# Kernel tuning notes

Measured on AMD Instinct MI355X. Metric: run time of the kernel, lower is better.

Reference implementation:

```python
import jax, jax.numpy as jnp
import numpy as np

N_NODES = 50000
N_EDGES = 800000
F_IN = 32
H = 128
N_REL = 4
MAX_DEG = 10
N_GRAPHS = 64
N_BLOCKS = 2


def setup_inputs() -> dict:
    key = jax.random.key(0)
    ks = jax.random.split(key, 20)
    s = 0.05
    return {
        "x": jax.random.normal(ks[0], (N_NODES, F_IN), jnp.float32),
        "edge_index": jax.random.randint(ks[1], (2, N_EDGES), 0, N_NODES, dtype=jnp.int32),
        "edge_attr": jax.random.randint(ks[2], (N_EDGES,), 0, N_REL, dtype=jnp.int32),
        "batch_idx": jnp.sort(jax.random.randint(ks[3], (N_NODES,), 0, N_GRAPHS, dtype=jnp.int32)),
        "embed_W": jax.random.normal(ks[4], (F_IN, H), jnp.float32) * s,
        "embed_b": jax.random.normal(ks[5], (H,), jnp.float32) * s,
        "rgcn_Wrel": jax.random.normal(ks[6], (N_BLOCKS, N_REL, H, H), jnp.float32) * s,
        "rgcn_Wroot": jax.random.normal(ks[7], (N_BLOCKS, H, H), jnp.float32) * s,
        "rgcn_b": jax.random.normal(ks[8], (N_BLOCKS, H), jnp.float32) * s,
        "mf_Wl": jax.random.normal(ks[9], (N_BLOCKS, MAX_DEG + 1, H, H), jnp.float32) * s,
        "mf_bl": jax.random.normal(ks[10], (N_BLOCKS, MAX_DEG + 1, H), jnp.float32) * s,
        "mf_Wr": jax.random.normal(ks[11], (N_BLOCKS, MAX_DEG + 1, H, H), jnp.float32) * s,
        "lin1_W": jax.random.normal(ks[12], (H, H), jnp.float32) * s,
        "lin1_b": jax.random.normal(ks[13], (H,), jnp.float32) * s,
        "lin2_W": jax.random.normal(ks[14], (H, 1), jnp.float32) * s,
        "lin2_b": jax.random.normal(ks[15], (1,), jnp.float32) * s,
    }


def _rgcn(x, src, dst, rel, Wrel, Wroot, b):
    # PyG RGCNConv with default aggr='mean': per-relation mean over incoming
    # edges, then per-relation weight, plus root transform and bias.
    seg = dst * N_REL + rel  # composite segment id: (node, relation)
    agg = jax.ops.segment_sum(x[src], seg, num_segments=N_NODES * N_REL)
    cnt = jax.ops.segment_sum(jnp.ones((seg.shape[0],), x.dtype), seg,
                              num_segments=N_NODES * N_REL)
    agg = (agg / jnp.maximum(cnt, 1.0)[:, None]).reshape(N_NODES, N_REL, H)
    return jnp.einsum('nrh,rho->no', agg, Wrel) + x @ Wroot + b


def _mfconv(x, src, dst, Wl, bl, Wr):
    # PyG MFConv: sum-aggregate neighbors, then per-degree-bucket linear heads
    # (degree = in-degree clamped to MAX_DEG); lin_r applied to root x (no bias).
    h = jax.ops.segment_sum(x[src], dst, num_segments=N_NODES)  # [N,H]
    deg = jax.ops.segment_sum(jnp.ones((src.shape[0],), jnp.int32), dst,
                              num_segments=N_NODES)
    deg = jnp.minimum(deg, MAX_DEG)  # [N]
    # out_all: [D+1, N, H] candidate outputs, one per degree bucket
    out_all = (jnp.einsum('nh,dho->dno', h, Wl)
               + jnp.einsum('nh,dho->dno', x, Wr)
               + bl[:, None, :])
    return jnp.take_along_axis(out_all, deg[None, :, None], axis=0)[0]


def reference(x, edge_index, edge_attr, batch_idx, embed_W, embed_b,
              rgcn_Wrel, rgcn_Wroot, rgcn_b, mf_Wl, mf_bl, mf_Wr,
              lin1_W, lin1_b, lin2_W, lin2_b):
    src, dst = edge_index[0], edge_index[1]
    h = x @ embed_W + embed_b
    for blk in range(N_BLOCKS):
        if blk > 0:  # first block uses Identity instead of ReLU
            h = jax.nn.relu(h)
        h = _rgcn(h, src, dst, edge_attr, rgcn_Wrel[blk], rgcn_Wroot[blk], rgcn_b[blk])
        h = jax.nn.relu(h)
        h = _mfconv(h, src, dst, mf_Wl[blk], mf_bl[blk], mf_Wr[blk])
    g = jax.ops.segment_sum(h, batch_idx, num_segments=N_GRAPHS)  # global_add_pool
    g = jax.nn.relu(g @ lin1_W + lin1_b)
    return g @ lin2_W + lin2_b
```

## Files before the change

kernel.cpp:

```cpp
#include <hip/hip_runtime.h>
#include <hip/hip_bf16.h>

#define NRELS 4
#define MAXDEG 10
#define NBUCK 11
#define POOL_CHUNKS 8

typedef __attribute__((ext_vector_type(8))) short s16x8;
typedef __attribute__((ext_vector_type(4))) float f32x4;
typedef __attribute__((ext_vector_type(8))) unsigned short u16x8;

__device__ inline unsigned short f2b(float f) {
  __hip_bfloat16 h = __float2bfloat16(f);
  return *reinterpret_cast<unsigned short*>(&h);
}
__device__ inline float b2f(unsigned short u) {
  union { unsigned int i; float f; } v;
  v.i = ((unsigned int)u) << 16;
  return v.f;
}
__device__ inline float blo(unsigned int v) {
  union { unsigned int i; float f; } x;
  x.i = v << 16;
  return x.f;
}
__device__ inline float bhi(unsigned int v) {
  union { unsigned int i; float f; } x;
  x.i = v & 0xffff0000u;
  return x.f;
}

typedef __attribute__((address_space(3))) unsigned int lds_uint;
typedef __attribute__((address_space(1))) const unsigned int glob_uint;
__device__ __forceinline__ void gld_lds16(const void* g, void* l) {
  __builtin_amdgcn_global_load_lds((glob_uint*)g, (lds_uint*)l, 16, 0, 0);
}

__global__ __launch_bounds__(512) void coarse_count_scan(
    const int* __restrict__ dst, int* __restrict__ bhist, int* __restrict__ boff,
    int* __restrict__ bcur, int* __restrict__ done, int* __restrict__ perm, int permCap,
    int NB, int E, int nblocks) {
  __shared__ int lh[512];
  __shared__ int lastf;
  int t = threadIdx.x;
  lh[t] = 0;
  __syncthreads();
  for (int i = blockIdx.x * 512 + t; i < permCap; i += nblocks * 512) perm[i] = -1;
  int base = blockIdx.x * 4096;
  int lim = E - base;
  if (lim > 4096) lim = 4096;
  for (int i = t; i < lim; i += 512) atomicAdd(&lh[dst[base + i] >> 7], 1);
  __syncthreads();
  if (lh[t]) atomicAdd(&bhist[t], lh[t]);
  __threadfence();
  __syncthreads();
  if (t == 0) lastf = (atomicAdd(done, 1) == nblocks - 1) ? 1 : 0;
  __syncthreads();
  if (!lastf) return;
  int v = (t < NB) ? atomicAdd(&bhist[t], 0) : 0;
  lh[t] = v;
  __syncthreads();
  for (int o = 1; o < 512; o <<= 1) {
    int x = (t >= o) ? lh[t - o] : 0;
    __syncthreads();
    lh[t] += x;
    __syncthreads();
  }
  if (t < NB) {
    int st = lh[t] - v;
    boff[t] = st;
    bcur[t] = st;
  }
  if (t == 0) boff[NB] = E;
}

__global__ __launch_bounds__(512) void coarse_scatter(
    const int* __restrict__ src, const int* __restrict__ dst, const int* __restrict__ rel,
    int* __restrict__ bcur, uint2* __restrict__ ebuf, int E) {
  __shared__ int lhist[512];
  __shared__ int lstart[512];
  __shared__ int lcur[512];
  __shared__ int gbase[512];
  __shared__ uint2 stage[4096];
  int t = threadIdx.x;
  lhist[t] = 0;
  __syncthreads();
  int base = blockIdx.x * 4096;
  int lim = E - base;
  if (lim > 4096) lim = 4096;
  for (int i = t; i < lim; i += 512) atomicAdd(&lhist[dst[base + i] >> 7], 1);
  __syncthreads();
  int myc = lhist[t];
  lstart[t] = myc;
  __syncthreads();
  for (int o = 1; o < 512; o <<= 1) {
    int x = (t >= o) ? lstart[t - o] : 0;
    __syncthreads();
    lstart[t] += x;
    __syncthreads();
  }
  int incl = lstart[t];
  __syncthreads();
  lstart[t] = incl - myc;
  lcur[t] = 0;
  if (myc > 0) gbase[t] = atomicAdd(&bcur[t], myc);
  __syncthreads();
  for (int i = t; i < lim; i += 512) {
    int e = base + i;
    int d = dst[e];
    int b = d >> 7;
    int slot = lstart[b] + atomicAdd(&lcur[b], 1);
    stage[slot] = make_uint2((unsigned)(d * 4 + rel[e]), (unsigned)src[e]);
  }
  __syncthreads();
  for (int i = t; i < lim; i += 512) {
    uint2 val = stage[i];
    int b = (int)(val.x >> 9);
    ebuf[gbase[b] + (i - lstart[b])] = val;
  }
}

__global__ __launch_bounds__(512) void fine_place(
    const uint2* __restrict__ ebuf, const int* __restrict__ boff, int* __restrict__ cnt,
    int* __restrict__ seg_start, float* __restrict__ inv, int* __restrict__ deg,
    int* __restrict__ bucket, int* __restrict__ hist, int* __restrict__ csr, int NSEG) {
  __shared__ int lh[512];
  __shared__ int sc[512];
  __shared__ int lcur[512];
  __shared__ int lbh[16];
  int t = threadIdx.x;
  int b = blockIdx.x;
  lh[t] = 0;
  if (t < 16) lbh[t] = 0;
  __syncthreads();
  int s = boff[b], e = boff[b + 1];
  for (int i = s + t; i < e; i += 512) atomicAdd(&lh[ebuf[i].x & 511], 1);
  __syncthreads();
  int v = lh[t];
  sc[t] = v;
  __syncthreads();
  for (int o = 1; o < 512; o <<= 1) {
    int x = (t >= o) ? sc[t - o] : 0;
    __syncthreads();
    sc[t] += x;
    __syncthreads();
  }
  int gseg = b * 512 + t;
  int mystart = s + sc[t] - v;
  lcur[t] = mystart;
  if (gseg < NSEG) {
    cnt[gseg] = v;
    seg_start[gseg] = mystart;
    inv[gseg] = 1.0f / (float)(v > 1 ? v : 1);
    if ((t & 3) == 0) {
      int d = sc[t + 3] - sc[t] + v;
      int n = gseg >> 2;
      deg[n] = d;
      int bk = d < MAXDEG ? d : MAXDEG;
      bucket[n] = bk;
      atomicAdd(&lbh[bk], 1);
    }
  }
  __syncthreads();
  if (t < NBUCK && lbh[t]) atomicAdd(&hist[t], lbh[t]);
  for (int i = s + t; i < e; i += 512) {
    uint2 vv = ebuf[i];
    int pos = atomicAdd(&lcur[vv.x & 511], 1);
    csr[pos] = (int)vv.y;
  }
}

__global__ void build_perm(const int* __restrict__ bucket, const int* __restrict__ hist,
                           int* __restrict__ fill, int* __restrict__ perm, int N) {
  __shared__ int soff[NBUCK];
  if (threadIdx.x == 0) {
    int acc = 0;
    for (int b = 0; b < NBUCK; b++) {
      soff[b] = acc;
      acc += ((hist[b] + 63) >> 6) << 6;
    }
  }
  __syncthreads();
  int n = blockIdx.x * 256 + threadIdx.x;
  int b = (n < N) ? bucket[n] : -1;
  int lane = threadIdx.x & 63;
  for (int bb = 0; bb < NBUCK; bb++) {
    unsigned long long m = __ballot(b == bb);
    if (m == 0ULL) continue;
    int leader = __ffsll(m) - 1;
    int base = 0;
    if (lane == leader) base = atomicAdd(&fill[bb], __popcll(m));
    base = __shfl(base, leader);
    if (b == bb) {
      int idx = __popcll(m & ((1ULL << lane) - 1ULL));
      perm[soff[bb] + base + idx] = n;
    }
  }
}

__global__ __launch_bounds__(256) void embed_conv(
    const float* __restrict__ x, const float* __restrict__ embW,
    const float* __restrict__ bias, const float* __restrict__ Wrel,
    const float* __restrict__ Wroot, const float* __restrict__ Wl,
    const float* __restrict__ Wr, unsigned short* __restrict__ Bt,
    unsigned short* __restrict__ Btm, unsigned short* __restrict__ out, int N, int nbE) {
  if ((int)blockIdx.x >= nbE) {
    const int R1 = 2 * 128 * 640;
    const int R2 = R1 + 2 * 11 * 128 * 256;
    int t = (blockIdx.x - nbE) * 256 + threadIdx.x;
    if (t < R1) {
      int blk = t / 81920;
      int rem = t % 81920;
      int n = rem / 640;
      int k = rem % 640;
      float v;
      if (k < 512)
        v = Wrel[(size_t)blk * 65536 + (size_t)k * 128 + n];
      else
        v = Wroot[(size_t)blk * 16384 + (size_t)(k - 512) * 128 + n];
      Bt[t] = f2b(v);
    } else if (t < R2) {
      int t2 = t - R1;
      int k = t2 & 255;
      int n = (t2 >> 8) & 127;
      int bb = (t2 >> 15) % 11;
      int blk = t2 / (11 * 128 * 256);
      float v;
      if (k < 128)
        v = Wl[(((size_t)blk * 11 + bb) * 128 + k) * 128 + n];
      else
        v = Wr[(((size_t)blk * 11 + bb) * 128 + (k - 128)) * 128 + n];
      Btm[t2] = f2b(v);
    }
    return;
  }
  __shared__ unsigned char As[64 * 80];
  __shared__ unsigned char Bs[128 * 80];
  int t = threadIdx.x;
  int m0 = blockIdx.x * 64;
  {
    int r = t >> 2, s = t & 3;
    int gr = m0 + r;
    if (gr >= N) gr = N - 1;
    const float* xp = x + (size_t)gr * 32 + s * 8;
    float4 f0 = *(const float4*)xp;
    float4 f1 = *(const float4*)(xp + 4);
    u16x8 o;
    o[0] = f2b(f0.x); o[1] = f2b(f0.y); o[2] = f2b(f0.z); o[3] = f2b(f0.w);
    o[4] = f2b(f1.x); o[5] = f2b(f1.y); o[6] = f2b(f1.z); o[7] = f2b(f1.w);
    *(u16x8*)(As + r * 80 + s * 16) = o;
  }
  {
    int n = t >> 1, hf = t & 1;
    unsigned short tmp[16];
#pragma unroll
    for (int j = 0; j < 16; j++) tmp[j] = f2b(embW[(size_t)(hf * 16 + j) * 128 + n]);
    *(u16x8*)(Bs + n * 80 + hf * 32) = *(u16x8*)tmp;
    *(u16x8*)(Bs + n * 80 + hf * 32 + 16) = *(u16x8*)(tmp + 8);
  }
  __syncthreads();
  int lane = t & 63, wave = t >> 6;
  int row = lane & 15, quad = lane >> 4;
  int nh = wave * 32;
  f32x4 acc[2][4];
#pragma unroll
  for (int i = 0; i < 2; i++)
#pragma unroll
    for (int j = 0; j < 4; j++) acc[i][j] = (f32x4){0.f, 0.f, 0.f, 0.f};
  s16x8 af[4], bf[2];
#pragma unroll
  for (int mt = 0; mt < 4; mt++) {
    int R = mt * 16 + row;
    af[mt] = *(const s16x8*)(As + R * 80 + quad * 16);
  }
#pragma unroll
  for (int nt = 0; nt < 2; nt++) {
    int R = nh + nt * 16 + row;
    bf[nt] = *(const s16x8*)(Bs + R * 80 + quad * 16);
  }
#pragma unroll
  for (int nt = 0; nt < 2; nt++)
#pragma unroll
    for (int mt = 0; mt < 4; mt++)
      acc[nt][mt] = __builtin_amdgcn_mfma_f32_16x16x32_bf16(af[mt], bf[nt], acc[nt][mt], 0, 0, 0);
#pragma unroll
  for (int nt = 0; nt < 2; nt++) {
    int n = nh + nt * 16 + row;
    float bv = bias[n];
#pragma unroll
    for (int mt = 0; mt < 4; mt++) {
#pragma unroll
      for (int r4 = 0; r4 < 4; r4++) {
        int m = m0 + mt * 16 + quad * 4 + r4;
        if (m < N) out[(size_t)m * 128 + n] = f2b(acc[nt][mt][r4] + bv);
      }
    }
  }
}

__device__ __forceinline__ void acc8v(float* a, uint4 v) {
  a[0] += blo(v.x); a[1] += bhi(v.x);
  a[2] += blo(v.y); a[3] += bhi(v.y);
  a[4] += blo(v.z); a[5] += bhi(v.z);
  a[6] += blo(v.w); a[7] += bhi(v.w);
}

__device__ __forceinline__ void gather_seg(const unsigned short* __restrict__ hb,
                                           const int* __restrict__ csr, int st, int cn,
                                           int chunk, float* a) {
  const unsigned short* hq = hb + chunk * 16;
  int i = 0;
  for (; i + 2 <= cn; i += 2) {
    int p0 = csr[st + i], p1 = csr[st + i + 1];
    const uint4* r0 = (const uint4*)(hq + (size_t)p0 * 128);
    const uint4* r1 = (const uint4*)(hq + (size_t)p1 * 128);
    uint4 v00 = r0[0], v01 = r0[1];
    uint4 v10 = r1[0], v11 = r1[1];
    acc8v(a + 0, v00); acc8v(a + 8, v01);
    acc8v(a + 0, v10); acc8v(a + 8, v11);
  }
  if (i < cn) {
    const uint4* r0 = (const uint4*)(hq + (size_t)csr[st + i] * 128);
    acc8v(a + 0, r0[0]); acc8v(a + 8, r0[1]);
  }
}

__device__ __forceinline__ void write_frag(unsigned char* Ag, int ln, int chunk,
                                           const float* a, float w) {
  int s = chunk >> 2;
#pragma unroll
  for (int h = 0; h < 2; h++) {
    int c = (((chunk & 3) * 2 + h)) ^ (ln & 7);
    const float* p = a + h * 8;
    uint4 o;
    o.x = (unsigned int)f2b(p[0] * w) | ((unsigned int)f2b(p[1] * w) << 16);
    o.y = (unsigned int)f2b(p[2] * w) | ((unsigned int)f2b(p[3] * w) << 16);
    o.z = (unsigned int)f2b(p[4] * w) | ((unsigned int)f2b(p[5] * w) << 16);
    o.w = (unsigned int)f2b(p[6] * w) | ((unsigned int)f2b(p[7] * w) << 16);
    *(uint4*)(Ag + s * 8192 + ln * 128 + (c << 4)) = o;
  }
}

__device__ __forceinline__ void gemm_tile_gB(const unsigned char* Areg, const char* Bp,
                                             int strideB, int row, int quad, int nh,
                                             f32x4 acc[2][4]) {
#pragma unroll
  for (int s = 0; s < 2; s++) {
#pragma unroll
    for (int ks = 0; ks < 2; ks++) {
      int cch = ks * 4 + quad;
      s16x8 af[4], bf[2];
#pragma unroll
      for (int mt = 0; mt < 4; mt++) {
        int R = mt * 16 + row;
        af[mt] = *(const s16x8*)(Areg + s * 8192 + R * 128 + ((cch ^ (R & 7)) << 4));
      }
#pragma unroll
      for (int nt = 0; nt < 2; nt++) {
        int R = nh + nt * 16 + row;
        bf[nt] = *(const s16x8*)(Bp + (size_t)R * strideB + s * 128 + cch * 16);
      }
#pragma unroll
      for (int nt = 0; nt < 2; nt++)
#pragma unroll
        for (int mt = 0; mt < 4; mt++)
          acc[nt][mt] = __builtin_amdgcn_mfma_f32_16x16x32_bf16(af[mt], bf[nt], acc[nt][mt], 0, 0, 0);
    }
  }
}

__global__ __launch_bounds__(256) void rgcn_fused(
    const unsigned short* __restrict__ hb, const int* __restrict__ csr,
    const int* __restrict__ seg_start, const int* __restrict__ cnt,
    const float* __restrict__ inv, const int* __restrict__ perm,
    const unsigned short* __restrict__ Bt, const float* __restrict__ bias,
    unsigned short* __restrict__ out) {
  __shared__ unsigned char Ag[16384];
  __shared__ int nodes[64];
  int t = threadIdx.x;
  int m0 = blockIdx.x * 64;
  if (t < 64) nodes[t] = perm[m0 + t];
  __syncthreads();
  int lane = t & 63, wave = t >> 6;
  int row = lane & 15, quad = lane >> 4;
  int nh = wave * 32;
  int chunk = t & 7, lnb = t >> 3;
  f32x4 acc[2][4];
#pragma unroll
  for (int i = 0; i < 2; i++)
#pragma unroll
    for (int j = 0; j < 4; j++) acc[i][j] = (f32x4){0.f, 0.f, 0.f, 0.f};

  for (int rel = 0; rel < 4; rel++) {
#pragma unroll
    for (int pp = 0; pp < 2; pp++) {
      int ln = pp * 32 + lnb;
      int nd = nodes[ln];
      float a[16];
#pragma unroll
      for (int j = 0; j < 16; j++) a[j] = 0.f;
      float w = 1.f;
      if (nd >= 0) {
        int sid = nd * 4 + rel;
        int st = seg_start[sid], cn2 = cnt[sid];
        w = inv[sid];
        gather_seg(hb, csr, st, cn2, chunk, a);
      }
      write_frag(Ag, ln, chunk, a, w);
    }
    __syncthreads();
    gemm_tile_gB(Ag, (const char*)Bt + rel * 256, 1280, row, quad, nh, acc);
    __syncthreads();
  }
#pragma unroll
  for (int s = 0; s < 2; s++)
#pragma unroll
    for (int p = 0; p < 2; p++) {
      int o = s * 8192 + p * 4096 + t * 16;
      int r = (o >> 7) & 63, c = ((o >> 4) & 7) ^ (r & 7);
      int nd = nodes[r];
      if (nd < 0) nd = 0;
      gld_lds16((const char*)hb + (size_t)nd * 256 + s * 128 + c * 16, Ag + o);
    }
  __syncthreads();
  gemm_tile_gB(Ag, (const char*)Bt + 1024, 1280, row, quad, nh, acc);
#pragma unroll
  for (int nt = 0; nt < 2; nt++) {
    int n = nh + nt * 16 + row;
    float bv = bias[n];
#pragma unroll
    for (int mt = 0; mt < 4; mt++) {
#pragma unroll
      for (int r4 = 0; r4 < 4; r4++) {
        int nd = nodes[mt * 16 + quad * 4 + r4];
        if (nd >= 0) out[(size_t)nd * 128 + n] = f2b(fmaxf(acc[nt][mt][r4] + bv, 0.f));
      }
    }
  }
}

__global__ __launch_bounds__(256) void mf_fused(
    const unsigned short* __restrict__ hb, const int* __restrict__ csr,
    const int* __restrict__ seg_start, const int* __restrict__ deg,
    const int* __restrict__ perm, const int* __restrict__ hist,
    const unsigned short* __restrict__ Bt, const float* __restrict__ bl,
    unsigned short* __restrict__ out, int relu_out) {
  __shared__ unsigned char Ag[16384];
  __shared__ int nodes[64];
  __shared__ int soff[NBUCK + 1];
  int t = threadIdx.x;
  int m0 = blockIdx.x * 64;
  if (t == 0) {
    int a2 = 0;
    for (int b2 = 0; b2 < NBUCK; b2++) {
      soff[b2] = a2;
      a2 += ((hist[b2] + 63) >> 6) << 6;
    }
    soff[NBUCK] = a2;
  }
  if (t < 64) nodes[t] = perm[m0 + t];
  __syncthreads();
  if (m0 >= soff[NBUCK]) return;
  int b = 0;
  while (b < 10 && m0 >= soff[b + 1]) b++;
  const char* Bb = (const char*)(Bt + (size_t)b * 128 * 256);
  int lane = t & 63, wave = t >> 6;
  int row = lane & 15, quad = lane >> 4;
  int nh = wave * 32;
  int chunk = t & 7, lnb = t >> 3;
  f32x4 acc[2][4];
#pragma unroll
  for (int i = 0; i < 2; i++)
#pragma unroll
    for (int j = 0; j < 4; j++) acc[i][j] = (f32x4){0.f, 0.f, 0.f, 0.f};
#pragma unroll
  for (int pp = 0; pp < 2; pp++) {
    int ln = pp * 32 + lnb;
    int nd = nodes[ln];
    float a[16];
#pragma unroll
    for (int j = 0; j < 16; j++) a[j] = 0.f;
    if (nd >= 0) gather_seg(hb, csr, seg_start[nd * 4], deg[nd], chunk, a);
    write_frag(Ag, ln, chunk, a, 1.f);
  }
  __syncthreads();
  gemm_tile_gB(Ag, Bb, 512, row, quad, nh, acc);
  __syncthreads();
#pragma unroll
  for (int s = 0; s < 2; s++)
#pragma unroll
    for (int p = 0; p < 2; p++) {
      int o = s * 8192 + p * 4096 + t * 16;
      int r = (o >> 7) & 63, c = ((o >> 4) & 7) ^ (r & 7);
      int nd = nodes[r];
      if (nd < 0) nd = 0;
      gld_lds16((const char*)hb + (size_t)nd * 256 + s * 128 + c * 16, Ag + o);
    }
  __syncthreads();
  gemm_tile_gB(Ag, Bb + 256, 512, row, quad, nh, acc);
  const float* bb = bl + b * 128;
#pragma unroll
  for (int nt = 0; nt < 2; nt++) {
    int n = nh + nt * 16 + row;
    float bv = bb[n];
#pragma unroll
    for (int mt = 0; mt < 4; mt++) {
#pragma unroll
      for (int r4 = 0; r4 < 4; r4++) {
        int nd = nodes[mt * 16 + quad * 4 + r4];
        if (nd >= 0) {
          float v = acc[nt][mt][r4] + bv;
          if (relu_out) v = fmaxf(v, 0.f);
          out[(size_t)nd * 128 + n] = f2b(v);
        }
      }
    }
  }
}

__global__ void pool2(const unsigned short* __restrict__ h, const int* __restrict__ batch,
                      float* __restrict__ g, int N, int G) {
  int gr = blockIdx.x / POOL_CHUNKS;
  int ck = blockIdx.x % POOL_CHUNKS;
  int t = threadIdx.x;
  int lane = t & 63, grp = t >> 6;
  int lo = 0, hi = N;
  while (lo < hi) {
    int m = (lo + hi) >> 1;
    if (batch[m] < gr) lo = m + 1; else hi = m;
  }
  int s = lo;
  lo = s; hi = N;
  while (lo < hi) {
    int m = (lo + hi) >> 1;
    if (batch[m] < gr + 1) lo = m + 1; else hi = m;
  }
  int e = lo;
  int len = e - s;
  int a = s + (int)(((long long)len * ck) / POOL_CHUNKS);
  int b = s + (int)(((long long)len * (ck + 1)) / POOL_CHUNKS);
  float s0 = 0.f, s1 = 0.f;
  for (int n = a + grp; n < b; n += 2) {
    unsigned int v = *(const unsigned int*)(h + (size_t)n * 128 + lane * 2);
    s0 += blo(v);
    s1 += bhi(v);
  }
  if (b > a + grp) {
    atomicAdd(&g[gr * 128 + lane * 2], s0);
    atomicAdd(&g[gr * 128 + lane * 2 + 1], s1);
  }
}

__global__ void head_kernel(const float* __restrict__ g, const float* __restrict__ W1,
                            const float* __restrict__ b1, const float* __restrict__ W2,
                            const float* __restrict__ b2, float* __restrict__ out) {
  int bg = blockIdx.x;
  int o = threadIdx.x;
  __shared__ float gs[128];
  __shared__ float red[128];
  gs[o] = g[bg * 128 + o];
  __syncthreads();
  float acc = b1[o];
  for (int k = 0; k < 128; k++) acc += gs[k] * W1[k * 128 + o];
  acc = fmaxf(acc, 0.f);
  red[o] = acc * W2[o];
  __syncthreads();
  for (int s = 64; s > 0; s >>= 1) {
    if (o < s) red[o] += red[o + s];
    __syncthreads();
  }
  if (o == 0) out[bg] = red[0] + b2[0];
}

extern "C" void kernel_launch(void* const* d_in, const int* in_sizes, int n_in,
                              void* d_out, int out_size, void* d_ws, size_t ws_size,
                              hipStream_t stream) {
  const float* x = (const float*)d_in[0];
  const int* ei = (const int*)d_in[1];
  const int* ea = (const int*)d_in[2];
  const int* batch = (const int*)d_in[3];
  const float* embW = (const float*)d_in[4];
  const float* embB = (const float*)d_in[5];
  const float* Wrel = (const float*)d_in[6];
  const float* Wroot = (const float*)d_in[7];
  const float* rb = (const float*)d_in[8];
  const float* Wl = (const float*)d_in[9];
  const float* bl = (const float*)d_in[10];
  const float* Wr = (const float*)d_in[11];
  const float* l1W = (const float*)d_in[12];
  const float* l1b = (const float*)d_in[13];
  const float* l2W = (const float*)d_in[14];
  const float* l2b = (const float*)d_in[15];
  float* out = (float*)d_out;

  int N = in_sizes[0] / 32;
  int E = in_sizes[2];
  int G = out_size;
  int NSEG = N * 4;
  int NB = (N + 127) >> 7;

  char* p = (char*)d_ws;
  auto alloc = [&](size_t bytes) {
    char* r = p;
    p += (bytes + 255) & ~(size_t)255;
    return r;
  };
  int permCap = ((N + 63) / 64 + NBUCK) * 64;
  unsigned short* h_bf = (unsigned short*)alloc((size_t)N * 128 * 2);
  unsigned short* h2_bf = (unsigned short*)alloc((size_t)N * 128 * 2);
  unsigned short* Btr = (unsigned short*)alloc((size_t)2 * 128 * 640 * 2);
  unsigned short* Btm = (unsigned short*)alloc((size_t)2 * 11 * 128 * 256 * 2);
  float* inv = (float*)alloc((size_t)NSEG * 4);
  int* cnt = (int*)alloc((size_t)NSEG * 4);
  int* seg_start = (int*)alloc((size_t)NSEG * 4);
  int* csr = (int*)alloc((size_t)E * 4);
  uint2* ebuf = (uint2*)alloc((size_t)E * 8);
  int* deg = (int*)alloc((size_t)N * 4);
  int* bucket = (int*)alloc((size_t)N * 4);
  int* perm = (int*)alloc((size_t)permCap * 4);
  int* boff = (int*)alloc(516 * 4);
  int* bcur = (int*)alloc(512 * 4);
  size_t zeroBytes = 8192 + (size_t)G * 128 * 4;
  char* zb = alloc(zeroBytes);
  int* bhist = (int*)zb;
  int* hist = (int*)(zb + 4096);
  int* fill = (int*)(zb + 4224);
  int* done = (int*)(zb + 4352);
  float* g = (float*)(zb + 8192);

  (void)hipMemsetAsync(zb, 0, zeroBytes, stream);

  const int* src = ei;
  const int* dst = ei + E;

  int sblocks = (E + 4095) / 4096;
  coarse_count_scan<<<sblocks, 512, 0, stream>>>(dst, bhist, boff, bcur, done, perm, permCap,
                                                 NB, E, sblocks);
  coarse_scatter<<<sblocks, 512, 0, stream>>>(src, dst, ea, bcur, ebuf, E);
  fine_place<<<NB, 512, 0, stream>>>(ebuf, boff, cnt, seg_start, inv, deg, bucket, hist, csr,
                                     NSEG);
  build_perm<<<(N + 255) / 256, 256, 0, stream>>>(bucket, hist, fill, perm, N);

  int nbE = (N + 63) / 64;
  int convBlocks = (2 * 128 * 640 + 2 * 11 * 128 * 256 + 255) / 256;
  embed_conv<<<nbE + convBlocks, 256, 0, stream>>>(x, embW, embB, Wrel, Wroot, Wl, Wr, Btr,
                                                   Btm, h_bf, N, nbE);

  int mfblocks = permCap / 64;
  for (int blk = 0; blk < 2; blk++) {
    rgcn_fused<<<mfblocks, 256, 0, stream>>>(h_bf, csr, seg_start, cnt, inv, perm,
                                             Btr + (size_t)blk * 81920, rb + blk * 128,
                                             h2_bf);
    mf_fused<<<mfblocks, 256, 0, stream>>>(h2_bf, csr, seg_start, deg, perm, hist,
                                           Btm + (size_t)blk * 11 * 128 * 256,
                                           bl + (size_t)blk * 11 * 128, h_bf,
                                           (blk == 0) ? 1 : 0);
  }
  pool2<<<G * POOL_CHUNKS, 128, 0, stream>>>(h_bf, batch, g, N, G);
  head_kernel<<<G, 128, 0, stream>>>(g, l1W, l1b, l2W, l2b, out);
}
```

Before: 406.2 us.

## Double LDS buffers to overlap neighbor gathers and root-row loads with GEMMs

In the RGCN kernel, two relations are gathered per iteration into separate LDS buffers, so one barrier pair covers two GEMM tiles and the segment metadata is read with vector loads. In the MFConv kernel, the async root-row load into a second LDS buffer is issued before the neighbor gather, and both GEMMs run after a single barrier. This cuts barrier count and hides global-load latency behind gather work. In exchange, LDS use per block doubles to about 32KB and register pressure rises from two live accumulator arrays, which may lower occupancy.

```diff
diff --git a/kernel.cpp b/kernel.cpp
--- a/kernel.cpp
+++ b/kernel.cpp
@@ -375,7 +375,8 @@
     const float* __restrict__ inv, const int* __restrict__ perm,
     const unsigned short* __restrict__ Bt, const float* __restrict__ bias,
     unsigned short* __restrict__ out) {
-  __shared__ unsigned char Ag[16384];
+  __shared__ unsigned char Ag0[16384];
+  __shared__ unsigned char Ag1[16384];
   __shared__ int nodes[64];
   int t = threadIdx.x;
   int m0 = blockIdx.x * 64;
@@ -391,25 +392,31 @@
 #pragma unroll
     for (int j = 0; j < 4; j++) acc[i][j] = (f32x4){0.f, 0.f, 0.f, 0.f};
 
-  for (int rel = 0; rel < 4; rel++) {
+#pragma unroll
+  for (int rp = 0; rp < 4; rp += 2) {
 #pragma unroll
     for (int pp = 0; pp < 2; pp++) {
       int ln = pp * 32 + lnb;
       int nd = nodes[ln];
-      float a[16];
-#pragma unroll
-      for (int j = 0; j < 16; j++) a[j] = 0.f;
-      float w = 1.f;
+      float a0[16], a1[16];
+#pragma unroll
+      for (int j = 0; j < 16; j++) { a0[j] = 0.f; a1[j] = 0.f; }
+      float w0 = 1.f, w1 = 1.f;
       if (nd >= 0) {
-        int sid = nd * 4 + rel;
-        int st = seg_start[sid], cn2 = cnt[sid];
-        w = inv[sid];
-        gather_seg(hb, csr, st, cn2, chunk, a);
+        int sb = nd * 4 + rp;
+        int2 st2 = *(const int2*)(seg_start + sb);
+        int2 cn2 = *(const int2*)(cnt + sb);
+        float2 w2 = *(const float2*)(inv + sb);
+        w0 = w2.x; w1 = w2.y;
+        gather_seg(hb, csr, st2.x, cn2.x, chunk, a0);
+        gather_seg(hb, csr, st2.y, cn2.y, chunk, a1);
       }
-      write_frag(Ag, ln, chunk, a, w);
-    }
-    __syncthreads();
-    gemm_tile_gB(Ag, (const char*)Bt + rel * 256, 1280, row, quad, nh, acc);
+      write_frag(Ag0, ln, chunk, a0, w0);
+      write_frag(Ag1, ln, chunk, a1, w1);
+    }
+    __syncthreads();
+    gemm_tile_gB(Ag0, (const char*)Bt + rp * 256, 1280, row, quad, nh, acc);
+    gemm_tile_gB(Ag1, (const char*)Bt + (rp + 1) * 256, 1280, row, quad, nh, acc);
     __syncthreads();
   }
 #pragma unroll
@@ -420,10 +427,10 @@
       int r = (o >> 7) & 63, c = ((o >> 4) & 7) ^ (r & 7);
       int nd = nodes[r];
       if (nd < 0) nd = 0;
-      gld_lds16((const char*)hb + (size_t)nd * 256 + s * 128 + c * 16, Ag + o);
-    }
-  __syncthreads();
-  gemm_tile_gB(Ag, (const char*)Bt + 1024, 1280, row, quad, nh, acc);
+      gld_lds16((const char*)hb + (size_t)nd * 256 + s * 128 + c * 16, Ag0 + o);
+    }
+  __syncthreads();
+  gemm_tile_gB(Ag0, (const char*)Bt + 1024, 1280, row, quad, nh, acc);
 #pragma unroll
   for (int nt = 0; nt < 2; nt++) {
     int n = nh + nt * 16 + row;
@@ -446,6 +453,7 @@
     const unsigned short* __restrict__ Bt, const float* __restrict__ bl,
     unsigned short* __restrict__ out, int relu_out) {
   __shared__ unsigned char Ag[16384];
+  __shared__ unsigned char Ar[16384];
   __shared__ int nodes[64];
   __shared__ int soff[NBUCK + 1];
   int t = threadIdx.x;
@@ -468,24 +476,6 @@
   int row = lane & 15, quad = lane >> 4;
   int nh = wave * 32;
   int chunk = t & 7, lnb = t >> 3;
-  f32x4 acc[2][4];
-#pragma unroll
-  for (int i = 0; i < 2; i++)
-#pragma unroll
-    for (int j = 0; j < 4; j++) acc[i][j] = (f32x4){0.f, 0.f, 0.f, 0.f};
-#pragma unroll
-  for (int pp = 0; pp < 2; pp++) {
-    int ln = pp * 32 + lnb;
-    int nd = nodes[ln];
-    float a[16];
-#pragma unroll
-    for (int j = 0; j < 16; j++) a[j] = 0.f;
-    if (nd >= 0) gather_seg(hb, csr, seg_start[nd * 4], deg[nd], chunk, a);
-    write_frag(Ag, ln, chunk, a, 1.f);
-  }
-  __syncthreads();
-  gemm_tile_gB(Ag, Bb, 512, row, quad, nh, acc);
-  __syncthreads();
 #pragma unroll
   for (int s = 0; s < 2; s++)
 #pragma unroll
@@ -494,10 +484,26 @@
       int r = (o >> 7) & 63, c = ((o >> 4) & 7) ^ (r & 7);
       int nd = nodes[r];
       if (nd < 0) nd = 0;
-      gld_lds16((const char*)hb + (size_t)nd * 256 + s * 128 + c * 16, Ag + o);
-    }
-  __syncthreads();
-  gemm_tile_gB(Ag, Bb + 256, 512, row, quad, nh, acc);
+      gld_lds16((const char*)hb + (size_t)nd * 256 + s * 128 + c * 16, Ar + o);
+    }
+  f32x4 acc[2][4];
+#pragma unroll
+  for (int i = 0; i < 2; i++)
+#pragma unroll
+    for (int j = 0; j < 4; j++) acc[i][j] = (f32x4){0.f, 0.f, 0.f, 0.f};
+#pragma unroll
+  for (int pp = 0; pp < 2; pp++) {
+    int ln = pp * 32 + lnb;
+    int nd = nodes[ln];
+    float a[16];
+#pragma unroll
+    for (int j = 0; j < 16; j++) a[j] = 0.f;
+    if (nd >= 0) gather_seg(hb, csr, seg_start[nd * 4], deg[nd], chunk, a);
+    write_frag(Ag, ln, chunk, a, 1.f);
+  }
+  __syncthreads();
+  gemm_tile_gB(Ag, Bb, 512, row, quad, nh, acc);
+  gemm_tile_gB(Ar, Bb + 256, 512, row, quad, nh, acc);
   const float* bb = bl + b * 128;
 #pragma unroll
   for (int nt = 0; nt < 2; nt++) {
```

Result: slower. 456.4 us (+12.4%).

## Interleave two-node neighbor gathers and use block-local histogram in build_perm

Applied to the files above, without the earlier changes.

The rgcn and mfconv gather phases now process both of a thread's node rows together, so eight neighbor-row loads are issued per iteration instead of four. This raises memory-level parallelism in the latency-bound gather. build_perm replaces the per-wave ballot loop over buckets with a shared-memory histogram and one global atomic per bucket per block. The global fill counters are padded to separate cache lines. The cost is higher register pressure from two 16-float accumulators per thread.

```diff
diff --git a/kernel.cpp b/kernel.cpp
--- a/kernel.cpp
+++ b/kernel.cpp
@@ -173,7 +173,11 @@
 __global__ void build_perm(const int* __restrict__ bucket, const int* __restrict__ hist,
                            int* __restrict__ fill, int* __restrict__ perm, int N) {
   __shared__ int soff[NBUCK];
-  if (threadIdx.x == 0) {
+  __shared__ int lh[NBUCK];
+  __shared__ int gbase[NBUCK];
+  int t = threadIdx.x;
+  if (t < NBUCK) lh[t] = 0;
+  if (t == 0) {
     int acc = 0;
     for (int b = 0; b < NBUCK; b++) {
       soff[b] = acc;
@@ -181,21 +185,16 @@
     }
   }
   __syncthreads();
-  int n = blockIdx.x * 256 + threadIdx.x;
-  int b = (n < N) ? bucket[n] : -1;
-  int lane = threadIdx.x & 63;
-  for (int bb = 0; bb < NBUCK; bb++) {
-    unsigned long long m = __ballot(b == bb);
-    if (m == 0ULL) continue;
-    int leader = __ffsll(m) - 1;
-    int base = 0;
-    if (lane == leader) base = atomicAdd(&fill[bb], __popcll(m));
-    base = __shfl(base, leader);
-    if (b == bb) {
-      int idx = __popcll(m & ((1ULL << lane) - 1ULL));
-      perm[soff[bb] + base + idx] = n;
-    }
-  }
+  int n = blockIdx.x * 256 + t;
+  int b = -1, lr = 0;
+  if (n < N) {
+    b = bucket[n];
+    lr = atomicAdd(&lh[b], 1);
+  }
+  __syncthreads();
+  if (t < NBUCK && lh[t] > 0) gbase[t] = atomicAdd(&fill[t * 16], lh[t]);
+  __syncthreads();
+  if (n < N) perm[soff[b] + gbase[b] + lr] = n;
 }
 
 __global__ __launch_bounds__(256) void embed_conv(
@@ -325,6 +324,31 @@
   }
 }
 
+__device__ __forceinline__ void gather2_seg(const unsigned short* __restrict__ hb,
+                                            const int* __restrict__ csr,
+                                            int st0, int cn0, int st1, int cn1,
+                                            int chunk, float* a0, float* a1) {
+  const unsigned short* hq = hb + chunk * 16;
+  int mn = cn0 < cn1 ? cn0 : cn1;
+  int i = 0;
+  for (; i + 2 <= mn; i += 2) {
+    int p00 = csr[st0 + i], p01 = csr[st0 + i + 1];
+    int p10 = csr[st1 + i], p11 = csr[st1 + i + 1];
+    const uint4* r00 = (const uint4*)(hq + (size_t)p00 * 128);
+    const uint4* r01 = (const uint4*)(hq + (size_t)p01 * 128);
+    const uint4* r10 = (const uint4*)(hq + (size_t)p10 * 128);
+    const uint4* r11 = (const uint4*)(hq + (size_t)p11 * 128);
+    uint4 v0a = r00[0], v0b = r00[1], v1a = r01[0], v1b = r01[1];
+    uint4 v2a = r10[0], v2b = r10[1], v3a = r11[0], v3b = r11[1];
+    acc8v(a0 + 0, v0a); acc8v(a0 + 8, v0b);
+    acc8v(a0 + 0, v1a); acc8v(a0 + 8, v1b);
+    acc8v(a1 + 0, v2a); acc8v(a1 + 8, v2b);
+    acc8v(a1 + 0, v3a); acc8v(a1 + 8, v3b);
+  }
+  if (i < cn0) gather_seg(hb, csr, st0 + i, cn0 - i, chunk, a0);
+  if (i < cn1) gather_seg(hb, csr, st1 + i, cn1 - i, chunk, a1);
+}
+
 __device__ __forceinline__ void write_frag(unsigned char* Ag, int ln, int chunk,
                                            const float* a, float w) {
   int s = chunk >> 2;
@@ -385,6 +409,8 @@
   int row = lane & 15, quad = lane >> 4;
   int nh = wave * 32;
   int chunk = t & 7, lnb = t >> 3;
+  int ln0 = lnb, ln1 = 32 + lnb;
+  int nd0 = nodes[ln0], nd1 = nodes[ln1];
   f32x4 acc[2][4];
 #pragma unroll
   for (int i = 0; i < 2; i++)
@@ -392,22 +418,22 @@
     for (int j = 0; j < 4; j++) acc[i][j] = (f32x4){0.f, 0.f, 0.f, 0.f};
 
   for (int rel = 0; rel < 4; rel++) {
-#pragma unroll
-    for (int pp = 0; pp < 2; pp++) {
-      int ln = pp * 32 + lnb;
-      int nd = nodes[ln];
-      float a[16];
-#pragma unroll
-      for (int j = 0; j < 16; j++) a[j] = 0.f;
-      float w = 1.f;
-      if (nd >= 0) {
-        int sid = nd * 4 + rel;
-        int st = seg_start[sid], cn2 = cnt[sid];
-        w = inv[sid];
-        gather_seg(hb, csr, st, cn2, chunk, a);
-      }
-      write_frag(Ag, ln, chunk, a, w);
-    }
+    float a0[16], a1[16];
+#pragma unroll
+    for (int j = 0; j < 16; j++) { a0[j] = 0.f; a1[j] = 0.f; }
+    int st0 = 0, cn0 = 0, st1 = 0, cn1 = 0;
+    float w0 = 1.f, w1 = 1.f;
+    if (nd0 >= 0) {
+      int sid = nd0 * 4 + rel;
+      st0 = seg_start[sid]; cn0 = cnt[sid]; w0 = inv[sid];
+    }
+    if (nd1 >= 0) {
+      int sid = nd1 * 4 + rel;
+      st1 = seg_start[sid]; cn1 = cnt[sid]; w1 = inv[sid];
+    }
+    gather2_seg(hb, csr, st0, cn0, st1, cn1, chunk, a0, a1);
+    write_frag(Ag, ln0, chunk, a0, w0);
+    write_frag(Ag, ln1, chunk, a1, w1);
     __syncthreads();
     gemm_tile_gB(Ag, (const char*)Bt + rel * 256, 1280, row, quad, nh, acc);
     __syncthreads();
@@ -468,20 +494,23 @@
   int row = lane & 15, quad = lane >> 4;
   int nh = wave * 32;
   int chunk = t & 7, lnb = t >> 3;
+  int ln0 = lnb, ln1 = 32 + lnb;
+  int nd0 = nodes[ln0], nd1 = nodes[ln1];
   f32x4 acc[2][4];
 #pragma unroll
   for (int i = 0; i < 2; i++)
 #pragma unroll
     for (int j = 0; j < 4; j++) acc[i][j] = (f32x4){0.f, 0.f, 0.f, 0.f};
-#pragma unroll
-  for (int pp = 0; pp < 2; pp++) {
-    int ln = pp * 32 + lnb;
-    int nd = nodes[ln];
-    float a[16];
-#pragma unroll
-    for (int j = 0; j < 16; j++) a[j] = 0.f;
-    if (nd >= 0) gather_seg(hb, csr, seg_start[nd * 4], deg[nd], chunk, a);
-    write_frag(Ag, ln, chunk, a, 1.f);
+  {
+    float a0[16], a1[16];
+#pragma unroll
+    for (int j = 0; j < 16; j++) { a0[j] = 0.f; a1[j] = 0.f; }
+    int st0 = 0, cn0 = 0, st1 = 0, cn1 = 0;
+    if (nd0 >= 0) { st0 = seg_start[nd0 * 4]; cn0 = deg[nd0]; }
+    if (nd1 >= 0) { st1 = seg_start[nd1 * 4]; cn1 = deg[nd1]; }
+    gather2_seg(hb, csr, st0, cn0, st1, cn1, chunk, a0, a1);
+    write_frag(Ag, ln0, chunk, a0, 1.f);
+    write_frag(Ag, ln1, chunk, a1, 1.f);
   }
   __syncthreads();
   gemm_tile_gB(Ag, Bb, 512, row, quad, nh, acc);
@@ -624,8 +653,8 @@
   char* zb = alloc(zeroBytes);
   int* bhist = (int*)zb;
   int* hist = (int*)(zb + 4096);
-  int* fill = (int*)(zb + 4224);
-  int* done = (int*)(zb + 4352);
+  int* fill = (int*)(zb + 4608);
+  int* done = (int*)(zb + 5376);
   float* g = (float*)(zb + 8192);
 
   (void)hipMemsetAsync(zb, 0, zeroBytes, stream);
```

Result: slower. 467.3 us (+15.0%).

## Shrink RGCN tile to 32 nodes, gather all relations before one GEMM phase

Applied to the files above, without the earlier changes.

The RGCN kernel now handles 32 nodes per block instead of 64. Each thread gathers all four relation segments into separate LDS buffers, and a single barrier is followed by four back-to-back GEMMs instead of a sync-gemm-sync cycle per relation. This removes per-relation barriers, lets gather loads from different relations overlap, and doubles the block count for latency hiding, at the cost of halving MFMA reuse of B fragments per block. build_perm also switches from per-wave ballots over buckets to an LDS histogram with one global atomic per bucket, and spaces the fill counters apart to reduce atomic contention.

```diff
diff --git a/kernel.cpp b/kernel.cpp
--- a/kernel.cpp
+++ b/kernel.cpp
@@ -173,7 +173,11 @@
 __global__ void build_perm(const int* __restrict__ bucket, const int* __restrict__ hist,
                            int* __restrict__ fill, int* __restrict__ perm, int N) {
   __shared__ int soff[NBUCK];
-  if (threadIdx.x == 0) {
+  __shared__ int lh[NBUCK];
+  __shared__ int gbase[NBUCK];
+  int t = threadIdx.x;
+  if (t < NBUCK) lh[t] = 0;
+  if (t == 0) {
     int acc = 0;
     for (int b = 0; b < NBUCK; b++) {
       soff[b] = acc;
@@ -181,21 +185,16 @@
     }
   }
   __syncthreads();
-  int n = blockIdx.x * 256 + threadIdx.x;
-  int b = (n < N) ? bucket[n] : -1;
-  int lane = threadIdx.x & 63;
-  for (int bb = 0; bb < NBUCK; bb++) {
-    unsigned long long m = __ballot(b == bb);
-    if (m == 0ULL) continue;
-    int leader = __ffsll(m) - 1;
-    int base = 0;
-    if (lane == leader) base = atomicAdd(&fill[bb], __popcll(m));
-    base = __shfl(base, leader);
-    if (b == bb) {
-      int idx = __popcll(m & ((1ULL << lane) - 1ULL));
-      perm[soff[bb] + base + idx] = n;
-    }
-  }
+  int n = blockIdx.x * 256 + t;
+  int b = -1, lr = 0;
+  if (n < N) {
+    b = bucket[n];
+    lr = atomicAdd(&lh[b], 1);
+  }
+  __syncthreads();
+  if (t < NBUCK && lh[t] > 0) gbase[t] = atomicAdd(&fill[t * 16], lh[t]);
+  __syncthreads();
+  if (n < N) perm[soff[b] + gbase[b] + lr] = n;
 }
 
 __global__ __launch_bounds__(256) void embed_conv(
@@ -341,6 +340,22 @@
   }
 }
 
+__device__ __forceinline__ void write_frag32(unsigned char* Ag, int ln, int chunk,
+                                             const float* a, float w) {
+  int s = chunk >> 2;
+#pragma unroll
+  for (int h = 0; h < 2; h++) {
+    int c = (((chunk & 3) * 2 + h)) ^ (ln & 7);
+    const float* p = a + h * 8;
+    uint4 o;
+    o.x = (unsigned int)f2b(p[0] * w) | ((unsigned int)f2b(p[1] * w) << 16);
+    o.y = (unsigned int)f2b(p[2] * w) | ((unsigned int)f2b(p[3] * w) << 16);
+    o.z = (unsigned int)f2b(p[4] * w) | ((unsigned int)f2b(p[5] * w) << 16);
+    o.w = (unsigned int)f2b(p[6] * w) | ((unsigned int)f2b(p[7] * w) << 16);
+    *(uint4*)(Ag + s * 4096 + ln * 128 + (c << 4)) = o;
+  }
+}
+
 __device__ __forceinline__ void gemm_tile_gB(const unsigned char* Areg, const char* Bp,
                                              int strideB, int row, int quad, int nh,
                                              f32x4 acc[2][4]) {
@@ -364,6 +379,34 @@
       for (int nt = 0; nt < 2; nt++)
 #pragma unroll
         for (int mt = 0; mt < 4; mt++)
+          acc[nt][mt] = __builtin_amdgcn_mfma_f32_16x16x32_bf16(af[mt], bf[nt], acc[nt][mt], 0, 0, 0);
+    }
+  }
+}
+
+__device__ __forceinline__ void gemm_tile32(const unsigned char* Areg, const char* Bp,
+                                            int strideB, int row, int quad, int nh,
+                                            f32x4 acc[2][2]) {
+#pragma unroll
+  for (int s = 0; s < 2; s++) {
+#pragma unroll
+    for (int ks = 0; ks < 2; ks++) {
+      int cch = ks * 4 + quad;
+      s16x8 af[2], bf[2];
+#pragma unroll
+      for (int mt = 0; mt < 2; mt++) {
+        int R = mt * 16 + row;
+        af[mt] = *(const s16x8*)(Areg + s * 4096 + R * 128 + ((cch ^ (R & 7)) << 4));
+      }
+#pragma unroll
+      for (int nt = 0; nt < 2; nt++) {
+        int R = nh + nt * 16 + row;
+        bf[nt] = *(const s16x8*)(Bp + (size_t)R * strideB + s * 128 + cch * 16);
+      }
+#pragma unroll
+      for (int nt = 0; nt < 2; nt++)
+#pragma unroll
+        for (int mt = 0; mt < 2; mt++)
           acc[nt][mt] = __builtin_amdgcn_mfma_f32_16x16x32_bf16(af[mt], bf[nt], acc[nt][mt], 0, 0, 0);
     }
   }
@@ -375,65 +418,61 @@
     const float* __restrict__ inv, const int* __restrict__ perm,
     const unsigned short* __restrict__ Bt, const float* __restrict__ bias,
     unsigned short* __restrict__ out) {
-  __shared__ unsigned char Ag[16384];
-  __shared__ int nodes[64];
+  __shared__ unsigned char At[4][8192];
+  __shared__ int nodes[32];
   int t = threadIdx.x;
-  int m0 = blockIdx.x * 64;
-  if (t < 64) nodes[t] = perm[m0 + t];
+  int m0 = blockIdx.x * 32;
+  if (t < 32) nodes[t] = perm[m0 + t];
   __syncthreads();
   int lane = t & 63, wave = t >> 6;
   int row = lane & 15, quad = lane >> 4;
   int nh = wave * 32;
-  int chunk = t & 7, lnb = t >> 3;
-  f32x4 acc[2][4];
+  int chunk = t & 7, ln = t >> 3;
+  int nd = nodes[ln];
+  f32x4 acc[2][2];
 #pragma unroll
   for (int i = 0; i < 2; i++)
 #pragma unroll
-    for (int j = 0; j < 4; j++) acc[i][j] = (f32x4){0.f, 0.f, 0.f, 0.f};
-
+    for (int j = 0; j < 2; j++) acc[i][j] = (f32x4){0.f, 0.f, 0.f, 0.f};
+
+#pragma unroll
   for (int rel = 0; rel < 4; rel++) {
-#pragma unroll
-    for (int pp = 0; pp < 2; pp++) {
-      int ln = pp * 32 + lnb;
-      int nd = nodes[ln];
-      float a[16];
-#pragma unroll
-      for (int j = 0; j < 16; j++) a[j] = 0.f;
-      float w = 1.f;
-      if (nd >= 0) {
-        int sid = nd * 4 + rel;
-        int st = seg_start[sid], cn2 = cnt[sid];
-        w = inv[sid];
-        gather_seg(hb, csr, st, cn2, chunk, a);
-      }
-      write_frag(Ag, ln, chunk, a, w);
-    }
-    __syncthreads();
-    gemm_tile_gB(Ag, (const char*)Bt + rel * 256, 1280, row, quad, nh, acc);
-    __syncthreads();
-  }
-#pragma unroll
-  for (int s = 0; s < 2; s++)
-#pragma unroll
-    for (int p = 0; p < 2; p++) {
-      int o = s * 8192 + p * 4096 + t * 16;
-      int r = (o >> 7) & 63, c = ((o >> 4) & 7) ^ (r & 7);
-      int nd = nodes[r];
-      if (nd < 0) nd = 0;
-      gld_lds16((const char*)hb + (size_t)nd * 256 + s * 128 + c * 16, Ag + o);
-    }
-  __syncthreads();
-  gemm_tile_gB(Ag, (const char*)Bt + 1024, 1280, row, quad, nh, acc);
+    float a[16];
+#pragma unroll
+    for (int j = 0; j < 16; j++) a[j] = 0.f;
+    float w = 1.f;
+    if (nd >= 0) {
+      int sid = nd * 4 + rel;
+      w = inv[sid];
+      gather_seg(hb, csr, seg_start[sid], cnt[sid], chunk, a);
+    }
+    write_frag32(At[rel], ln, chunk, a, w);
+  }
+  __syncthreads();
+#pragma unroll
+  for (int rel = 0; rel < 4; rel++)
+    gemm_tile32(At[rel], (const char*)Bt + rel * 256, 1280, row, quad, nh, acc);
+  __syncthreads();
+#pragma unroll
+  for (int s = 0; s < 2; s++) {
+    int o = s * 4096 + t * 16;
+    int r = t >> 3, c = (t & 7) ^ (r & 7);
+    int nd2 = nodes[r];
+    if (nd2 < 0) nd2 = 0;
+    gld_lds16((const char*)hb + (size_t)nd2 * 256 + s * 128 + c * 16, At[0] + o);
+  }
+  __syncthreads();
+  gemm_tile32(At[0], (const char*)Bt + 1024, 1280, row, quad, nh, acc);
 #pragma unroll
   for (int nt = 0; nt < 2; nt++) {
     int n = nh + nt * 16 + row;
     float bv = bias[n];
 #pragma unroll
-    for (int mt = 0; mt < 4; mt++) {
+    for (int mt = 0; mt < 2; mt++) {
 #pragma unroll
       for (int r4 = 0; r4 < 4; r4++) {
-        int nd = nodes[mt * 16 + quad * 4 + r4];
-        if (nd >= 0) out[(size_t)nd * 128 + n] = f2b(fmaxf(acc[nt][mt][r4] + bv, 0.f));
+        int nd3 = nodes[mt * 16 + quad * 4 + r4];
+        if (nd3 >= 0) out[(size_t)nd3 * 128 + n] = f2b(fmaxf(acc[nt][mt][r4] + bv, 0.f));
       }
     }
   }
@@ -624,8 +663,8 @@
   char* zb = alloc(zeroBytes);
   int* bhist = (int*)zb;
   int* hist = (int*)(zb + 4096);
-  int* fill = (int*)(zb + 4224);
-  int* done = (int*)(zb + 4352);
+  int* fill = (int*)(zb + 4608);
+  int* done = (int*)(zb + 5376);
   float* g = (float*)(zb + 8192);
 
   (void)hipMemsetAsync(zb, 0, zeroBytes, stream);
@@ -646,11 +685,12 @@
   embed_conv<<<nbE + convBlocks, 256, 0, stream>>>(x, embW, embB, Wrel, Wroot, Wl, Wr, Btr,
                                                    Btm, h_bf, N, nbE);
 
+  int rgcnBlocks = permCap / 32;
   int mfblocks = permCap / 64;
   for (int blk = 0; blk < 2; blk++) {
-    rgcn_fused<<<mfblocks, 256, 0, stream>>>(h_bf, csr, seg_start, cnt, inv, perm,
-                                             Btr + (size_t)blk * 81920, rb + blk * 128,
-                                             h2_bf);
+    rgcn_fused<<<rgcnBlocks, 256, 0, stream>>>(h_bf, csr, seg_start, cnt, inv, perm,
+                                               Btr + (size_t)blk * 81920, rb + blk * 128,
+                                               h2_bf);
     mf_fused<<<mfblocks, 256, 0, stream>>>(h2_bf, csr, seg_start, deg, perm, hist,
                                            Btm + (size_t)blk * 11 * 128 * 256,
                                            bl + (size_t)blk * 11 * 128, h_bf,
```

Result: slower. 417.5 us (+2.8%).
